# Performance work log

Measured on AMD Instinct MI355X. Metric: run time of the kernel, lower is better.

Reference implementation:

```python
import jax, jax.numpy as jnp
import numpy as np
import math

B, T, D, H, V, L = 8, 512, 128, 512, 50257, 8
DT = 1.0
RAW_INIT = math.log(math.expm1(1.0))  # so softplus(raw) == 1.0


def setup_inputs() -> dict:
    key = jax.random.key(0)
    ks = jax.random.split(key, 8)
    x = jax.random.randint(ks[0], (B, T), 0, V)
    E = jax.random.normal(ks[1], (V, D), jnp.float32) * 0.02
    P = jax.random.normal(ks[2], (T, D), jnp.float32) * 0.01
    W0 = jax.random.normal(ks[3], (2 * D, H), jnp.float32) * 0.02
    W1 = jax.random.normal(ks[4], (H, H), jnp.float32) * 0.02
    W2 = jax.random.normal(ks[5], (H, H), jnp.float32) * 0.02
    W3 = jax.random.normal(ks[6], (H, 1), jnp.float32) * 0.002
    return {
        'x': x, 'E': E, 'P': P,
        'W0': W0, 'b0': jnp.zeros((H,), jnp.float32),
        'W1': W1, 'b1': jnp.zeros((H,), jnp.float32),
        'W2': W2, 'b2': jnp.zeros((H,), jnp.float32),
        'W3': W3, 'b3': jnp.zeros((1,), jnp.float32),
        'raw_m_bias': jnp.asarray(RAW_INIT, jnp.float32),
        'raw_gamma': jnp.asarray(RAW_INIT, jnp.float32),
    }


def causal_cumulative_mean(h):
    t = h.shape[1]
    denom = jnp.arange(1, t + 1, dtype=h.dtype)[None, :, None]
    return jnp.cumsum(h, axis=1) / denom


def mlp_energy_sum(xi, h, W0, b0, W1, b1, W2, b2, W3, b3):
    z = jnp.concatenate([xi, h], axis=-1)  # (B,T,2D)
    z = jax.nn.gelu(z @ W0 + b0, approximate=False)
    z = jax.nn.gelu(z @ W1 + b1, approximate=False)
    z = jax.nn.gelu(z @ W2 + b2, approximate=False)
    return jnp.sum(z @ W3 + b3)


def reference(x, E, P, W0, b0, W1, b1, W2, b2, W3, b3, raw_m_bias, raw_gamma):
    emb = E[x] + P[None, :T]  # (B,T,D)
    gamma = jax.nn.softplus(raw_gamma)
    m = jax.nn.softplus(raw_m_bias) + 0.001  # global mass
    h = emb
    v = jnp.zeros_like(h)
    for _ in range(L):
        # causal_force=True: xi built from detached h
        xi = causal_cumulative_mean(jax.lax.stop_gradient(h))
        grad_V = jax.grad(
            lambda hh: mlp_energy_sum(xi, hh, W0, b0, W1, b1, W2, b2, W3, b3)
        )(h)
        f = -grad_V
        v = (v + DT * f / m) / (1.0 + DT * gamma)
        h = h + DT * v
    logits = jnp.einsum('btd,vd->btv', h, E)  # (B,T,V)
    return logits
```

## Files before the change

### kernel.cpp

```cpp
#include <hip/hip_runtime.h>
#include <hip/hip_bf16.h>

typedef __attribute__((ext_vector_type(8))) short short8;
typedef __attribute__((ext_vector_type(4))) float f32x4;
typedef unsigned char u8;

#define DEV static __device__ __forceinline__

DEV void gelu_pair(float x, float& z, float& dz){
  float ax = fabsf(x)*0.70710678118654752f;
  float e  = __expf(-ax*ax);
  float t  = __fdividef(1.0f, 1.0f + 0.3275911f*ax);
  float poly = t*(0.254829592f + t*(-0.284496736f + t*(1.421413741f +
               t*(-1.453152027f + t*1.061405429f))));
  float erfv = 1.0f - poly*e;
  erfv = x < 0.0f ? -erfv : erfv;
  float cdf = 0.5f*(1.0f + erfv);
  z  = x*cdf;
  dz = cdf + x*0.39894228040143268f*e;
}
DEV float dgelu_f(float x){ float zz, dz; gelu_pair(x, zz, dz); return dz; }
DEV float softplus_f(float x){ return log1pf(expf(x)); }
DEV void store_f4_a4(float* p, f32x4 v){ __builtin_memcpy(p, &v, 16); }

DEV void gload_lds16(const __hip_bfloat16* g, __hip_bfloat16* l){
  __builtin_amdgcn_global_load_lds((const __attribute__((address_space(1))) void*)g,
                                   (__attribute__((address_space(3))) void*)l, 16, 0, 0);
}

DEV u8 f2fp8(float f){
  int r = __builtin_amdgcn_cvt_pk_fp8_f32(f, f, 0, false);
  return (u8)(r & 0xff);
}
DEV unsigned pk4_fp8(float a, float b, float c, float d){
  int r = __builtin_amdgcn_cvt_pk_fp8_f32(a, b, 0, false);
  r = __builtin_amdgcn_cvt_pk_fp8_f32(c, d, r, true);
  return (unsigned)r;
}

DEV unsigned pack2bf(float a, float b){
  __hip_bfloat16 ba = __float2bfloat16(a), bb = __float2bfloat16(b);
  unsigned short ua, ub;
  __builtin_memcpy(&ua, &ba, 2); __builtin_memcpy(&ub, &bb, 2);
  return (unsigned)ua | ((unsigned)ub << 16);
}
DEV float unp_lo(unsigned u){ union{unsigned x; float f;} c; c.x = u << 16; return c.f; }
DEV float unp_hi(unsigned u){ union{unsigned x; float f;} c; c.x = u & 0xffff0000u; return c.f; }

#define SW    32.0f
#define SZC   32.0f
#define SZ1   256.0f
#define SZ2   1024.0f
#define SG3   256.0f
#define INV1  (1.0f/1024.0f)
#define INV2  (1.0f/8192.0f)
#define INV3  (1.0f/32768.0f)
#define INV4  (1.0f/8192.0f)
#define EN4   0.125f
#define INV5  (1.0f/32768.0f)
#define EN5   0.125f
#define INV6  (1.0f/131072.0f)

__global__ __launch_bounds__(512) void embed_k(const int* __restrict__ x,
                        const float* __restrict__ E, const float* __restrict__ P,
                        float* __restrict__ h, float* __restrict__ S){
  int bid = blockIdx.x;
  int row = threadIdx.x >> 5;
  int q   = threadIdx.x & 31;
  int tok = bid*16 + row;
  int t   = tok & 511;
  int id  = x[tok];
  float4 e4 = ((const float4*)E)[(size_t)id*32 + q];
  float4 p4 = ((const float4*)P)[(size_t)t*32 + q];
  float4 val; val.x=e4.x+p4.x; val.y=e4.y+p4.y; val.z=e4.z+p4.z; val.w=e4.w+p4.w;
  ((float4*)h)[(size_t)tok*32 + q] = val;
  __shared__ float4 ps[16][32];
  ps[row][q] = val;
  __syncthreads();
  if (row==0){
    float4 s = ps[0][q];
    #pragma unroll
    for (int r=1;r<16;r++){
      float4 t4 = ps[r][q];
      s.x+=t4.x; s.y+=t4.y; s.z+=t4.z; s.w+=t4.w;
    }
    ((float4*)S)[(size_t)bid*32 + q] = s;
  }
}

__global__ void convw_k(const float* __restrict__ W0, const float* __restrict__ W1,
                        const float* __restrict__ W2,
                        u8* __restrict__ W0T, u8* __restrict__ W1T,
                        u8* __restrict__ W2T, u8* __restrict__ W2b,
                        u8* __restrict__ W1b, u8* __restrict__ W0h){
  int i = blockIdx.x*256 + threadIdx.x;
  if (i < 131072){
    int e=i&7, n=(i>>3)&511, kk=i>>12; int k=(kk>>2)*32+(kk&3)*8+e;
    W0T[i]=f2fp8(SW*W0[(size_t)k*512+n]);
  } else if (i < 393216){
    int j=i-131072; int e=j&7, n=(j>>3)&511, kk=j>>12; int k=(kk>>2)*32+(kk&3)*8+e;
    W1T[j]=f2fp8(SW*W1[(size_t)k*512+n]);
  } else if (i < 655360){
    int j=i-393216; int e=j&7, n=(j>>3)&511, kk=j>>12; int k=(kk>>2)*32+(kk&3)*8+e;
    W2T[j]=f2fp8(SW*W2[(size_t)k*512+n]);
  } else if (i < 917504){
    int j=i-655360; int e=j&7, n=(j>>3)&511, kk=j>>12; int k=(kk>>2)*32+(kk&3)*8+e;
    W2b[j]=f2fp8(SW*W2[(size_t)n*512+k]);
  } else if (i < 1179648){
    int j=i-917504; int e=j&7, n=(j>>3)&511, kk=j>>12; int k=(kk>>2)*32+(kk&3)*8+e;
    W1b[j]=f2fp8(SW*W1[(size_t)n*512+k]);
  } else if (i < 1245184){
    int j=i-1179648; int e=j&7, n=(j>>3)&127, kk=j>>10; int k=(kk>>2)*32+(kk&3)*8+e;
    W0h[j]=f2fp8(SW*W0[(size_t)(128+n)*512+k]);
  }
}
__global__ void conv_c4_k(const float* __restrict__ W, __hip_bfloat16* __restrict__ Wb, int n4){
  int i = blockIdx.x*256 + threadIdx.x;
  if (i < n4){
    float4 f = ((const float4*)W)[i];
    Wb[4*i+0]=__float2bfloat16(f.x);
    Wb[4*i+1]=__float2bfloat16(f.y);
    Wb[4*i+2]=__float2bfloat16(f.z);
    Wb[4*i+3]=__float2bfloat16(f.w);
  }
}

struct LayerP {
  const u8 *W0T,*W1T,*W2T,*W2b,*W1b,*W0h;
  const float *b0,*b1,*b2,*W3;
  float *v, *h; __hip_bfloat16* hbf;
  const float* Sprev; float* Snext;
  const float *rawm,*rawg;
  int first, last;
};

template<int KSTEPS, int NW, int NF>
DEV void wpre(const u8* __restrict__ Wt, int nbase, int r16, int g, int rot,
              long (&bb)[6][NF]){
  const u8* wp = Wt + ((size_t)g*NW + nbase + r16)*8;
  #pragma unroll
  for (int d=0; d<5; d++){
    if (d < KSTEPS){
      int dd = (d + rot) & (KSTEPS-1);
      #pragma unroll
      for (int f=0; f<NF; f++)
        bb[d][f] = *(const long*)&wp[((size_t)dd*4*NW + (size_t)f*16)*8];
    }
  }
}

template<int KSTEPS, int NW, int NF>
DEV void gphase(const u8* __restrict__ Wt,
                const u8* __restrict__ zin,
                int nbase, int r16, int g, int rot, f32x4 (&acc)[NF],
                long (&bb)[6][NF]){
  #pragma unroll
  for (int f=0;f<NF;f++) acc[f] = (f32x4){0.f,0.f,0.f,0.f};
  const u8* wp = Wt + ((size_t)g*NW + nbase + r16)*8;
  #pragma unroll
  for (int s=0; s<KSTEPS; s++){
    if (s+5 < KSTEPS){
      int ss5 = (s + 5 + rot) & (KSTEPS-1);
      const u8* wn = wp + (size_t)ss5*4*NW*8;
      #pragma unroll
      for (int f=0; f<NF; f++)
        bb[(s+5)%6][f] = *(const long*)&wn[(size_t)f*128];
    }
    int ss = (s + rot) & (KSTEPS-1);
    long a = *(const long*)&zin[(ss*4+g)*128 + r16*8];
    #pragma unroll
    for (int f=0; f<NF; f++)
      acc[f] = __builtin_amdgcn_mfma_f32_16x16x32_fp8_fp8(a, bb[s%6][f], acc[f],0,0,0);
  }
}

__global__ __launch_bounds__(1024,4) void layer_k(LayerP p){
  __shared__ __align__(16) u8 sZ[2][8192];
  __shared__ float4 psum[16][32];
  __shared__ float4 psumC[16][32];
  const int tid = threadIdx.x;
  const int w = tid >> 6, lane = tid & 63;
  const int r16 = lane & 15, g = lane >> 4;
  const int rb = blockIdx.x;
  const int nb = w*32;
  const int rot = (rb >> 3) & 15;

  long bb[6][2];

  wpre<8,512,2>(p.W0T, nb, r16, g, rot, bb);
  float vr[4] = {0.f,0.f,0.f,0.f}, hr[4] = {0.f,0.f,0.f,0.f};
  float im = 0.f, fac = 0.f;
  if (w < 8){
    const int col = w*16 + r16;
    #pragma unroll
    for (int j=0;j<4;j++){
      size_t o = ((size_t)rb*16 + g*4 + j)*128 + col;
      hr[j] = p.h[o];
      vr[j] = p.first ? 0.f : p.v[o];
    }
    im  = INV6/(softplus_f(p.rawm[0]) + 0.001f);
    fac = 1.0f/(1.0f + softplus_f(p.rawg[0]));
  }

  if (tid < 512){
    const int row = tid >> 5;
    const int lane32 = tid & 31;
    const int b = rb >> 5, c = rb & 31;
    const float4* S4 = (const float4*)(p.Sprev + (size_t)b*32*128) + lane32;
    float4 part = {0.f,0.f,0.f,0.f};
    if (row < c){
      float4 t = S4[(size_t)row*32];
      part.x+=t.x; part.y+=t.y; part.z+=t.z; part.w+=t.w;
    }
    if (row+16 < c){
      float4 t = S4[(size_t)(row+16)*32];
      part.x+=t.x; part.y+=t.y; part.z+=t.z; part.w+=t.w;
    }
    float4 myrow = ((const float4*)(p.h + (size_t)rb*16*128))[(size_t)row*32 + lane32];
    psum[row][lane32]  = myrow;
    psumC[row][lane32] = part;
    __syncthreads();
    float4 pfx = {0.f,0.f,0.f,0.f};
    #pragma unroll
    for (int r=0;r<16;r++){
      float4 t = psumC[r][lane32];
      pfx.x+=t.x; pfx.y+=t.y; pfx.z+=t.z; pfx.w+=t.w;
    }
    #pragma unroll
    for (int rr=0; rr<15; rr++){
      float4 t = psum[rr][lane32];
      float sel = rr < row ? 1.0f : 0.0f;
      pfx.x += sel*t.x; pfx.y += sel*t.y; pfx.z += sel*t.z; pfx.w += sel*t.w;
    }
    pfx.x+=myrow.x; pfx.y+=myrow.y; pfx.z+=myrow.z; pfx.w+=myrow.w;
    float inv32 = SZC/(float)(c*16 + row + 1);
    const int d0 = lane32*4;
    unsigned ux = pk4_fp8(pfx.x*inv32, pfx.y*inv32, pfx.z*inv32, pfx.w*inv32);
    unsigned uh = pk4_fp8(myrow.x*SZC, myrow.y*SZC, myrow.z*SZC, myrow.w*SZC);
    *(unsigned*)&sZ[0][(d0>>3)*128      + row*8 + (d0&7)] = ux;
    *(unsigned*)&sZ[0][(16+(d0>>3))*128 + row*8 + (d0&7)] = uh;
  } else {
    __syncthreads();
  }
  __syncthreads();

  f32x4 acc[2];
  unsigned g1p[2][2], g2p[2][2];

  gphase<8,512,2>(p.W0T, sZ[0], nb, r16, g, rot, acc, bb);
  wpre<16,512,2>(p.W1T, nb, r16, g, rot, bb);
  #pragma unroll
  for (int f=0; f<2; f++){
    int n = nb + f*16 + r16;
    float bias = p.b0[n];
    #pragma unroll
    for (int jp=0; jp<2; jp++){
      float z0, dz0, z1v, dz1;
      gelu_pair(acc[f][2*jp]*INV1   + bias, z0,  dz0);
      gelu_pair(acc[f][2*jp+1]*INV1 + bias, z1v, dz1);
      g1p[f][jp] = pack2bf(dz0, dz1);
      sZ[1][(n>>3)*128 + (g*4+2*jp)*8   + (n&7)] = f2fp8(z0*SZ1);
      sZ[1][(n>>3)*128 + (g*4+2*jp+1)*8 + (n&7)] = f2fp8(z1v*SZ1);
    }
  }
  __syncthreads();

  gphase<16,512,2>(p.W1T, sZ[1], nb, r16, g, rot, acc, bb);
  wpre<16,512,2>(p.W2T, nb, r16, g, rot, bb);
  #pragma unroll
  for (int f=0; f<2; f++){
    int n = nb + f*16 + r16;
    float bias = p.b1[n];
    #pragma unroll
    for (int jp=0; jp<2; jp++){
      float z0, dz0, z1v, dz1;
      gelu_pair(acc[f][2*jp]*INV2   + bias, z0,  dz0);
      gelu_pair(acc[f][2*jp+1]*INV2 + bias, z1v, dz1);
      g2p[f][jp] = pack2bf(dz0, dz1);
      sZ[0][(n>>3)*128 + (g*4+2*jp)*8   + (n&7)] = f2fp8(z0*SZ2);
      sZ[0][(n>>3)*128 + (g*4+2*jp+1)*8 + (n&7)] = f2fp8(z1v*SZ2);
    }
  }
  __syncthreads();

  gphase<16,512,2>(p.W2T, sZ[0], nb, r16, g, rot, acc, bb);
  wpre<16,512,2>(p.W2b, nb, r16, g, rot, bb);
  #pragma unroll
  for (int f=0; f<2; f++){
    int n = nb + f*16 + r16;
    float bias = p.b2[n];
    float w3s = p.W3[n]*SG3;
    #pragma unroll
    for (int j=0;j<4;j++){
      float xx = acc[f][j]*INV3 + bias;
      sZ[1][(n>>3)*128 + (g*4+j)*8 + (n&7)] = f2fp8(w3s*dgelu_f(xx));
    }
  }
  __syncthreads();

  gphase<16,512,2>(p.W2b, sZ[1], nb, r16, g, rot, acc, bb);
  wpre<16,512,2>(p.W1b, nb, r16, g, rot, bb);
  #pragma unroll
  for (int f=0; f<2; f++){
    int n = nb + f*16 + r16;
    #pragma unroll
    for (int jp=0; jp<2; jp++){
      float gv0 = unp_lo(g2p[f][jp]), gv1 = unp_hi(g2p[f][jp]);
      sZ[0][(n>>3)*128 + (g*4+2*jp)*8   + (n&7)] = f2fp8(acc[f][2*jp]*gv0*EN4);
      sZ[0][(n>>3)*128 + (g*4+2*jp+1)*8 + (n&7)] = f2fp8(acc[f][2*jp+1]*gv1*EN4);
    }
  }
  __syncthreads();

  gphase<16,512,2>(p.W1b, sZ[0], nb, r16, g, rot, acc, bb);
  long bbF[6][1];
  if (w < 8) wpre<16,128,1>(p.W0h, w*16, r16, g, rot, bbF);
  #pragma unroll
  for (int f=0; f<2; f++){
    int n = nb + f*16 + r16;
    #pragma unroll
    for (int jp=0; jp<2; jp++){
      float gv0 = unp_lo(g1p[f][jp]), gv1 = unp_hi(g1p[f][jp]);
      sZ[1][(n>>3)*128 + (g*4+2*jp)*8   + (n&7)] = f2fp8(acc[f][2*jp]*gv0*EN5);
      sZ[1][(n>>3)*128 + (g*4+2*jp+1)*8 + (n&7)] = f2fp8(acc[f][2*jp+1]*gv1*EN5);
    }
  }
  __syncthreads();

  if (w < 8){
    f32x4 accF[1];
    gphase<16,128,1>(p.W0h, sZ[1], w*16, r16, g, rot, accF, bbF);
    int col = w*16 + r16;
    float hs = 0.f;
    #pragma unroll
    for (int j=0;j<4;j++){
      int row = g*4 + j;
      size_t o = ((size_t)rb*16 + row)*128 + col;
      float nv = (vr[j] - accF[0][j]*im)*fac;
      float nh = hr[j] + nv;
      if (!p.last){ p.v[o] = nv; p.h[o] = nh; }
      else        { p.hbf[o] = __float2bfloat16(nh); }
      hs += nh;
    }
    if (!p.last){
      hs += __shfl_xor(hs, 16);
      hs += __shfl_xor(hs, 32);
      if (g==0) p.Snext[(size_t)rb*128 + col] = hs;
    }
  }
}

__global__ __launch_bounds__(256,4) void logits_k(const __hip_bfloat16* __restrict__ A,
                                                  const __hip_bfloat16* __restrict__ Bt,
                                                  float* __restrict__ out){
  constexpr int V = 50257;
  __shared__ __align__(16) __hip_bfloat16 sA[128*64];
  __shared__ __align__(16) __hip_bfloat16 sB[128*64];
  const int tid = threadIdx.x, lane = tid & 63, wave = tid >> 6;
  const int wg = ((blockIdx.x & 7) * 1572) + (blockIdx.x >> 3);
  const int mt = wg & 31, nt = wg >> 5;
  const int m0 = mt*128, n0 = nt*128;
  const int wm = (wave>>1)*64, wn = (wave&1)*64;
  const int r16 = lane & 15, g = lane >> 4;
  const int srow = tid >> 3;
  const int scol = ((tid & 7) ^ (srow & 7)) * 8;
  const int sx = (r16 & 7) * 8;
  f32x4 zero = {0.f,0.f,0.f,0.f};
  f32x4 acc[4][4];
  #pragma unroll
  for (int i=0;i<4;i++){ acc[i][0]=zero; acc[i][1]=zero; acc[i][2]=zero; acc[i][3]=zero; }

  auto stageA = [&](int ks){
    #pragma unroll
    for (int i=0;i<4;i++)
      gload_lds16(A + (size_t)(m0 + i*32 + srow)*128 + ks*64 + scol,
                  &sA[i*2048 + wave*512]);
  };
  auto stageB = [&](int ks){
    #pragma unroll
    for (int i=0;i<4;i++){
      int r = n0 + i*32 + srow; if (r > V-1) r = V-1;
      gload_lds16(Bt + (size_t)r*128 + ks*64 + scol,
                  &sB[i*2048 + wave*512]);
    }
  };
  stageA(0); stageB(0);
  __syncthreads();
  #pragma unroll
  for (int ks=0; ks<2; ks++){
    #pragma unroll
    for (int kk=0; kk<2; kk++){
      const int ko = kk*32 + g*8;
      short8 a[4], b[4];
      #pragma unroll
      for (int ti=0; ti<4; ti++) a[ti] = *(const short8*)&sA[(wm + ti*16 + r16)*64 + (ko ^ sx)];
      #pragma unroll
      for (int tj=0; tj<4; tj++) b[tj] = *(const short8*)&sB[(wn + tj*16 + r16)*64 + (ko ^ sx)];
      #pragma unroll
      for (int tb=0; tb<4; tb++)
        #pragma unroll
        for (int ta=0; ta<4; ta++)
          acc[tb][ta] = __builtin_amdgcn_mfma_f32_16x16x32_bf16(b[tb],a[ta],acc[tb][ta],0,0,0);
    }
    if (ks==0){
      __syncthreads();
      stageA(1); stageB(1);
      __syncthreads();
    }
  }
  #pragma unroll
  for (int tb=0; tb<4; tb++){
    #pragma unroll
    for (int ta=0; ta<4; ta++){
      int row = m0 + wm + ta*16 + r16;
      int n   = n0 + wn + tb*16 + g*4;
      f32x4 c = acc[tb][ta];
      float* po = out + (size_t)row*V + n;
      if (n + 3 < V){
        store_f4_a4(po, c);
      } else {
        #pragma unroll
        for (int j=0;j<4;j++) if (n+j < V) po[j] = c[j];
      }
    }
  }
}

extern "C" void kernel_launch(void* const* d_in, const int* in_sizes, int n_in,
                              void* d_out, int out_size, void* d_ws, size_t ws_size,
                              hipStream_t stream){
  const int*   x    = (const int*)  d_in[0];
  const float* E    = (const float*)d_in[1];
  const float* P    = (const float*)d_in[2];
  const float* W0   = (const float*)d_in[3];
  const float* b0   = (const float*)d_in[4];
  const float* W1   = (const float*)d_in[5];
  const float* b1   = (const float*)d_in[6];
  const float* W2   = (const float*)d_in[7];
  const float* b2   = (const float*)d_in[8];
  const float* W3   = (const float*)d_in[9];
  const float* rawm = (const float*)d_in[11];
  const float* rawg = (const float*)d_in[12];

  constexpr int B=8, T=512, D=128, H=512, V=50257, L=8;
  const int M = B*T;

  char* w = (char*)d_ws;
  auto alloc = [&](size_t bytes)->char*{ char* r = w; w += (bytes + 255) & ~(size_t)255; return r; };
  float* h            = (float*)alloc((size_t)M*D*4);
  float* v            = (float*)alloc((size_t)M*D*4);
  __hip_bfloat16* hbf = (__hip_bfloat16*)alloc((size_t)M*D*2);
  float* S0           = (float*)alloc((size_t)B*32*128*4);
  float* S1           = (float*)alloc((size_t)B*32*128*4);
  u8* W0T             = (u8*)alloc((size_t)131072);
  u8* W1T             = (u8*)alloc((size_t)262144);
  u8* W2T             = (u8*)alloc((size_t)262144);
  u8* W2b             = (u8*)alloc((size_t)262144);
  u8* W1b             = (u8*)alloc((size_t)262144);
  u8* W0h             = (u8*)alloc((size_t)65536);
  __hip_bfloat16* Ebf = (__hip_bfloat16*)alloc((size_t)V*D*2);

  convw_k  <<<4864, 256, 0, stream>>>(W0, W1, W2, W0T, W1T, W2T, W2b, W1b, W0h);
  conv_c4_k<<<(V*D/4+255)/256, 256, 0, stream>>>(E, Ebf, V*D/4);
  embed_k<<<M/16, 512, 0, stream>>>(x, E, P, h, S0);

  LayerP lp{};
  lp.W0T=W0T; lp.W1T=W1T; lp.W2T=W2T; lp.W2b=W2b; lp.W1b=W1b; lp.W0h=W0h;
  lp.b0=b0; lp.b1=b1; lp.b2=b2; lp.W3=W3;
  lp.v=v; lp.h=h; lp.hbf=hbf; lp.rawm=rawm; lp.rawg=rawg;

  for (int l=0; l<L; l++){
    lp.Sprev = (l&1) ? S1 : S0;
    lp.Snext = (l&1) ? S0 : S1;
    lp.first = (l==0) ? 1 : 0;
    lp.last  = (l==L-1) ? 1 : 0;
    layer_k<<<M/16, 1024, 0, stream>>>(lp);
  }
  logits_k<<<12576, 256, 0, stream>>>(hbf, Ebf, (float*)d_out);
}
```

Before: 540.7 us.

## Fuse embedding and all layers into one persistent kernel with grid barrier

Replaces the embed kernel and the eight per-layer launches with a single persistent kernel of 256 blocks. The blocks synchronise between layers through an atomic grid barrier and keep h and v resident in shared memory instead of round-tripping them through global memory. This removes launch gaps and global h/v traffic. It relies on all 256 blocks being co-resident, otherwise the barrier deadlocks, and it adds spin-wait cost at each barrier.

```diff
diff --git a/kernel.cpp b/kernel.cpp
--- a/kernel.cpp
+++ b/kernel.cpp
@@ -55,45 +55,18 @@
 #define INV1  (1.0f/1024.0f)
 #define INV2  (1.0f/8192.0f)
 #define INV3  (1.0f/32768.0f)
-#define INV4  (1.0f/8192.0f)
 #define EN4   0.125f
-#define INV5  (1.0f/32768.0f)
 #define EN5   0.125f
 #define INV6  (1.0f/131072.0f)
-
-__global__ __launch_bounds__(512) void embed_k(const int* __restrict__ x,
-                        const float* __restrict__ E, const float* __restrict__ P,
-                        float* __restrict__ h, float* __restrict__ S){
-  int bid = blockIdx.x;
-  int row = threadIdx.x >> 5;
-  int q   = threadIdx.x & 31;
-  int tok = bid*16 + row;
-  int t   = tok & 511;
-  int id  = x[tok];
-  float4 e4 = ((const float4*)E)[(size_t)id*32 + q];
-  float4 p4 = ((const float4*)P)[(size_t)t*32 + q];
-  float4 val; val.x=e4.x+p4.x; val.y=e4.y+p4.y; val.z=e4.z+p4.z; val.w=e4.w+p4.w;
-  ((float4*)h)[(size_t)tok*32 + q] = val;
-  __shared__ float4 ps[16][32];
-  ps[row][q] = val;
-  __syncthreads();
-  if (row==0){
-    float4 s = ps[0][q];
-    #pragma unroll
-    for (int r=1;r<16;r++){
-      float4 t4 = ps[r][q];
-      s.x+=t4.x; s.y+=t4.y; s.z+=t4.z; s.w+=t4.w;
-    }
-    ((float4*)S)[(size_t)bid*32 + q] = s;
-  }
-}
 
 __global__ void convw_k(const float* __restrict__ W0, const float* __restrict__ W1,
                         const float* __restrict__ W2,
                         u8* __restrict__ W0T, u8* __restrict__ W1T,
                         u8* __restrict__ W2T, u8* __restrict__ W2b,
-                        u8* __restrict__ W1b, u8* __restrict__ W0h){
+                        u8* __restrict__ W1b, u8* __restrict__ W0h,
+                        int* __restrict__ bar){
   int i = blockIdx.x*256 + threadIdx.x;
+  if (i == 0) bar[0] = 0;
   if (i < 131072){
     int e=i&7, n=(i>>3)&511, kk=i>>12; int k=(kk>>2)*32+(kk&3)*8+e;
     W0T[i]=f2fp8(SW*W0[(size_t)k*512+n]);
@@ -125,14 +98,26 @@
   }
 }
 
-struct LayerP {
+struct MegaP {
+  const int* x; const float* E; const float* P;
   const u8 *W0T,*W1T,*W2T,*W2b,*W1b,*W0h;
   const float *b0,*b1,*b2,*W3;
-  float *v, *h; __hip_bfloat16* hbf;
-  const float* Sprev; float* Snext;
+  __hip_bfloat16* hbf;
+  float *S0, *S1;
   const float *rawm,*rawg;
-  int first, last;
+  int* bar;
 };
+
+DEV void grid_bar(int* bar, int target){
+  __syncthreads();
+  if (threadIdx.x == 0){
+    __threadfence();
+    __hip_atomic_fetch_add(bar, 1, __ATOMIC_ACQ_REL, __HIP_MEMORY_SCOPE_AGENT);
+    while (__hip_atomic_load(bar, __ATOMIC_ACQUIRE, __HIP_MEMORY_SCOPE_AGENT) < target)
+      __builtin_amdgcn_s_sleep(2);
+  }
+  __syncthreads();
+}
 
 template<int KSTEPS, int NW, int NF>
 DEV void wpre(const u8* __restrict__ Wt, int nbase, int r16, int g, int rot,
@@ -174,178 +159,215 @@
   }
 }
 
-__global__ __launch_bounds__(1024,4) void layer_k(LayerP p){
+__global__ __launch_bounds__(1024,4) void mega_k(MegaP p){
   __shared__ __align__(16) u8 sZ[2][8192];
   __shared__ float4 psum[16][32];
   __shared__ float4 psumC[16][32];
+  __shared__ float  sVv[2048];
   const int tid = threadIdx.x;
   const int w = tid >> 6, lane = tid & 63;
   const int r16 = lane & 15, g = lane >> 4;
   const int rb = blockIdx.x;
   const int nb = w*32;
   const int rot = (rb >> 3) & 15;
+  const int bt = rb >> 5, c = rb & 31;
 
   long bb[6][2];
-
   wpre<8,512,2>(p.W0T, nb, r16, g, rot, bb);
-  float vr[4] = {0.f,0.f,0.f,0.f}, hr[4] = {0.f,0.f,0.f,0.f};
-  float im = 0.f, fac = 0.f;
-  if (w < 8){
-    const int col = w*16 + r16;
-    #pragma unroll
-    for (int j=0;j<4;j++){
-      size_t o = ((size_t)rb*16 + g*4 + j)*128 + col;
-      hr[j] = p.h[o];
-      vr[j] = p.first ? 0.f : p.v[o];
-    }
-    im  = INV6/(softplus_f(p.rawm[0]) + 0.001f);
-    fac = 1.0f/(1.0f + softplus_f(p.rawg[0]));
-  }
+
+  const float im  = INV6/(softplus_f(p.rawm[0]) + 0.001f);
+  const float fac = 1.0f/(1.0f + softplus_f(p.rawg[0]));
 
   if (tid < 512){
-    const int row = tid >> 5;
-    const int lane32 = tid & 31;
-    const int b = rb >> 5, c = rb & 31;
-    const float4* S4 = (const float4*)(p.Sprev + (size_t)b*32*128) + lane32;
-    float4 part = {0.f,0.f,0.f,0.f};
-    if (row < c){
-      float4 t = S4[(size_t)row*32];
-      part.x+=t.x; part.y+=t.y; part.z+=t.z; part.w+=t.w;
-    }
-    if (row+16 < c){
-      float4 t = S4[(size_t)(row+16)*32];
-      part.x+=t.x; part.y+=t.y; part.z+=t.z; part.w+=t.w;
-    }
-    float4 myrow = ((const float4*)(p.h + (size_t)rb*16*128))[(size_t)row*32 + lane32];
-    psum[row][lane32]  = myrow;
-    psumC[row][lane32] = part;
-    __syncthreads();
-    float4 pfx = {0.f,0.f,0.f,0.f};
-    #pragma unroll
-    for (int r=0;r<16;r++){
-      float4 t = psumC[r][lane32];
-      pfx.x+=t.x; pfx.y+=t.y; pfx.z+=t.z; pfx.w+=t.w;
-    }
-    #pragma unroll
-    for (int rr=0; rr<15; rr++){
-      float4 t = psum[rr][lane32];
-      float sel = rr < row ? 1.0f : 0.0f;
-      pfx.x += sel*t.x; pfx.y += sel*t.y; pfx.z += sel*t.z; pfx.w += sel*t.w;
-    }
-    pfx.x+=myrow.x; pfx.y+=myrow.y; pfx.z+=myrow.z; pfx.w+=myrow.w;
-    float inv32 = SZC/(float)(c*16 + row + 1);
-    const int d0 = lane32*4;
-    unsigned ux = pk4_fp8(pfx.x*inv32, pfx.y*inv32, pfx.z*inv32, pfx.w*inv32);
-    unsigned uh = pk4_fp8(myrow.x*SZC, myrow.y*SZC, myrow.z*SZC, myrow.w*SZC);
-    *(unsigned*)&sZ[0][(d0>>3)*128      + row*8 + (d0&7)] = ux;
-    *(unsigned*)&sZ[0][(16+(d0>>3))*128 + row*8 + (d0&7)] = uh;
-  } else {
-    __syncthreads();
+    int row = tid >> 5, lane32 = tid & 31;
+    int tok = rb*16 + row, t = tok & 511;
+    int id = p.x[tok];
+    float4 e4 = ((const float4*)p.E)[(size_t)id*32 + lane32];
+    float4 p4 = ((const float4*)p.P)[(size_t)t*32 + lane32];
+    float4 val; val.x=e4.x+p4.x; val.y=e4.y+p4.y; val.z=e4.z+p4.z; val.w=e4.w+p4.w;
+    psum[row][lane32] = val;
   }
   __syncthreads();
+  if (tid < 32){
+    float4 s = psum[0][tid];
+    #pragma unroll
+    for (int r=1;r<16;r++){
+      float4 t4 = psum[r][tid];
+      s.x+=t4.x; s.y+=t4.y; s.z+=t4.z; s.w+=t4.w;
+    }
+    float* d = p.S0 + (size_t)rb*128 + tid*4;
+    __hip_atomic_store(d+0, s.x, __ATOMIC_RELAXED, __HIP_MEMORY_SCOPE_AGENT);
+    __hip_atomic_store(d+1, s.y, __ATOMIC_RELAXED, __HIP_MEMORY_SCOPE_AGENT);
+    __hip_atomic_store(d+2, s.z, __ATOMIC_RELAXED, __HIP_MEMORY_SCOPE_AGENT);
+    __hip_atomic_store(d+3, s.w, __ATOMIC_RELAXED, __HIP_MEMORY_SCOPE_AGENT);
+  }
+  grid_bar(p.bar, 256);
 
   f32x4 acc[2];
   unsigned g1p[2][2], g2p[2][2];
 
-  gphase<8,512,2>(p.W0T, sZ[0], nb, r16, g, rot, acc, bb);
-  wpre<16,512,2>(p.W1T, nb, r16, g, rot, bb);
-  #pragma unroll
-  for (int f=0; f<2; f++){
-    int n = nb + f*16 + r16;
-    float bias = p.b0[n];
-    #pragma unroll
-    for (int jp=0; jp<2; jp++){
-      float z0, dz0, z1v, dz1;
-      gelu_pair(acc[f][2*jp]*INV1   + bias, z0,  dz0);
-      gelu_pair(acc[f][2*jp+1]*INV1 + bias, z1v, dz1);
-      g1p[f][jp] = pack2bf(dz0, dz1);
-      sZ[1][(n>>3)*128 + (g*4+2*jp)*8   + (n&7)] = f2fp8(z0*SZ1);
-      sZ[1][(n>>3)*128 + (g*4+2*jp+1)*8 + (n&7)] = f2fp8(z1v*SZ1);
-    }
-  }
-  __syncthreads();
-
-  gphase<16,512,2>(p.W1T, sZ[1], nb, r16, g, rot, acc, bb);
-  wpre<16,512,2>(p.W2T, nb, r16, g, rot, bb);
-  #pragma unroll
-  for (int f=0; f<2; f++){
-    int n = nb + f*16 + r16;
-    float bias = p.b1[n];
-    #pragma unroll
-    for (int jp=0; jp<2; jp++){
-      float z0, dz0, z1v, dz1;
-      gelu_pair(acc[f][2*jp]*INV2   + bias, z0,  dz0);
-      gelu_pair(acc[f][2*jp+1]*INV2 + bias, z1v, dz1);
-      g2p[f][jp] = pack2bf(dz0, dz1);
-      sZ[0][(n>>3)*128 + (g*4+2*jp)*8   + (n&7)] = f2fp8(z0*SZ2);
-      sZ[0][(n>>3)*128 + (g*4+2*jp+1)*8 + (n&7)] = f2fp8(z1v*SZ2);
-    }
-  }
-  __syncthreads();
-
-  gphase<16,512,2>(p.W2T, sZ[0], nb, r16, g, rot, acc, bb);
-  wpre<16,512,2>(p.W2b, nb, r16, g, rot, bb);
-  #pragma unroll
-  for (int f=0; f<2; f++){
-    int n = nb + f*16 + r16;
-    float bias = p.b2[n];
-    float w3s = p.W3[n]*SG3;
-    #pragma unroll
-    for (int j=0;j<4;j++){
-      float xx = acc[f][j]*INV3 + bias;
-      sZ[1][(n>>3)*128 + (g*4+j)*8 + (n&7)] = f2fp8(w3s*dgelu_f(xx));
-    }
-  }
-  __syncthreads();
-
-  gphase<16,512,2>(p.W2b, sZ[1], nb, r16, g, rot, acc, bb);
-  wpre<16,512,2>(p.W1b, nb, r16, g, rot, bb);
-  #pragma unroll
-  for (int f=0; f<2; f++){
-    int n = nb + f*16 + r16;
-    #pragma unroll
-    for (int jp=0; jp<2; jp++){
-      float gv0 = unp_lo(g2p[f][jp]), gv1 = unp_hi(g2p[f][jp]);
-      sZ[0][(n>>3)*128 + (g*4+2*jp)*8   + (n&7)] = f2fp8(acc[f][2*jp]*gv0*EN4);
-      sZ[0][(n>>3)*128 + (g*4+2*jp+1)*8 + (n&7)] = f2fp8(acc[f][2*jp+1]*gv1*EN4);
-    }
-  }
-  __syncthreads();
-
-  gphase<16,512,2>(p.W1b, sZ[0], nb, r16, g, rot, acc, bb);
-  long bbF[6][1];
-  if (w < 8) wpre<16,128,1>(p.W0h, w*16, r16, g, rot, bbF);
-  #pragma unroll
-  for (int f=0; f<2; f++){
-    int n = nb + f*16 + r16;
-    #pragma unroll
-    for (int jp=0; jp<2; jp++){
-      float gv0 = unp_lo(g1p[f][jp]), gv1 = unp_hi(g1p[f][jp]);
-      sZ[1][(n>>3)*128 + (g*4+2*jp)*8   + (n&7)] = f2fp8(acc[f][2*jp]*gv0*EN5);
-      sZ[1][(n>>3)*128 + (g*4+2*jp+1)*8 + (n&7)] = f2fp8(acc[f][2*jp+1]*gv1*EN5);
-    }
-  }
-  __syncthreads();
-
-  if (w < 8){
-    f32x4 accF[1];
-    gphase<16,128,1>(p.W0h, sZ[1], w*16, r16, g, rot, accF, bbF);
-    int col = w*16 + r16;
-    float hs = 0.f;
-    #pragma unroll
-    for (int j=0;j<4;j++){
-      int row = g*4 + j;
-      size_t o = ((size_t)rb*16 + row)*128 + col;
-      float nv = (vr[j] - accF[0][j]*im)*fac;
-      float nh = hr[j] + nv;
-      if (!p.last){ p.v[o] = nv; p.h[o] = nh; }
-      else        { p.hbf[o] = __float2bfloat16(nh); }
-      hs += nh;
-    }
-    if (!p.last){
-      hs += __shfl_xor(hs, 16);
-      hs += __shfl_xor(hs, 32);
-      if (g==0) p.Snext[(size_t)rb*128 + col] = hs;
+  #pragma unroll 1
+  for (int l=0; l<8; l++){
+    const float* Sp = (l&1) ? p.S1 : p.S0;
+    float*       Sn = (l&1) ? p.S0 : p.S1;
+
+    if (tid < 512){
+      const int row = tid >> 5;
+      const int lane32 = tid & 31;
+      float4 part = {0.f,0.f,0.f,0.f};
+      const float* Sb = Sp + (size_t)bt*32*128 + lane32*4;
+      if (row < c){
+        const float* q4 = Sb + (size_t)row*128;
+        part.x += __hip_atomic_load(q4+0, __ATOMIC_RELAXED, __HIP_MEMORY_SCOPE_AGENT);
+        part.y += __hip_atomic_load(q4+1, __ATOMIC_RELAXED, __HIP_MEMORY_SCOPE_AGENT);
+        part.z += __hip_atomic_load(q4+2, __ATOMIC_RELAXED, __HIP_MEMORY_SCOPE_AGENT);
+        part.w += __hip_atomic_load(q4+3, __ATOMIC_RELAXED, __HIP_MEMORY_SCOPE_AGENT);
+      }
+      if (row+16 < c){
+        const float* q4 = Sb + (size_t)(row+16)*128;
+        part.x += __hip_atomic_load(q4+0, __ATOMIC_RELAXED, __HIP_MEMORY_SCOPE_AGENT);
+        part.y += __hip_atomic_load(q4+1, __ATOMIC_RELAXED, __HIP_MEMORY_SCOPE_AGENT);
+        part.z += __hip_atomic_load(q4+2, __ATOMIC_RELAXED, __HIP_MEMORY_SCOPE_AGENT);
+        part.w += __hip_atomic_load(q4+3, __ATOMIC_RELAXED, __HIP_MEMORY_SCOPE_AGENT);
+      }
+      float4 myrow = psum[row][lane32];
+      psumC[row][lane32] = part;
+      __syncthreads();
+      float4 pfx = {0.f,0.f,0.f,0.f};
+      #pragma unroll
+      for (int r=0;r<16;r++){
+        float4 t = psumC[r][lane32];
+        pfx.x+=t.x; pfx.y+=t.y; pfx.z+=t.z; pfx.w+=t.w;
+      }
+      #pragma unroll
+      for (int rr=0; rr<15; rr++){
+        float4 t = psum[rr][lane32];
+        float sel = rr < row ? 1.0f : 0.0f;
+        pfx.x += sel*t.x; pfx.y += sel*t.y; pfx.z += sel*t.z; pfx.w += sel*t.w;
+      }
+      pfx.x+=myrow.x; pfx.y+=myrow.y; pfx.z+=myrow.z; pfx.w+=myrow.w;
+      float inv32 = SZC/(float)(c*16 + row + 1);
+      const int d0 = lane32*4;
+      unsigned ux = pk4_fp8(pfx.x*inv32, pfx.y*inv32, pfx.z*inv32, pfx.w*inv32);
+      unsigned uh = pk4_fp8(myrow.x*SZC, myrow.y*SZC, myrow.z*SZC, myrow.w*SZC);
+      *(unsigned*)&sZ[0][(d0>>3)*128      + row*8 + (d0&7)] = ux;
+      *(unsigned*)&sZ[0][(16+(d0>>3))*128 + row*8 + (d0&7)] = uh;
+    } else {
+      __syncthreads();
+    }
+    __syncthreads();
+
+    gphase<8,512,2>(p.W0T, sZ[0], nb, r16, g, rot, acc, bb);
+    wpre<16,512,2>(p.W1T, nb, r16, g, rot, bb);
+    #pragma unroll
+    for (int f=0; f<2; f++){
+      int n = nb + f*16 + r16;
+      float bias = p.b0[n];
+      #pragma unroll
+      for (int jp=0; jp<2; jp++){
+        float z0, dz0, z1v, dz1;
+        gelu_pair(acc[f][2*jp]*INV1   + bias, z0,  dz0);
+        gelu_pair(acc[f][2*jp+1]*INV1 + bias, z1v, dz1);
+        g1p[f][jp] = pack2bf(dz0, dz1);
+        sZ[1][(n>>3)*128 + (g*4+2*jp)*8   + (n&7)] = f2fp8(z0*SZ1);
+        sZ[1][(n>>3)*128 + (g*4+2*jp+1)*8 + (n&7)] = f2fp8(z1v*SZ1);
+      }
+    }
+    __syncthreads();
+
+    gphase<16,512,2>(p.W1T, sZ[1], nb, r16, g, rot, acc, bb);
+    wpre<16,512,2>(p.W2T, nb, r16, g, rot, bb);
+    #pragma unroll
+    for (int f=0; f<2; f++){
+      int n = nb + f*16 + r16;
+      float bias = p.b1[n];
+      #pragma unroll
+      for (int jp=0; jp<2; jp++){
+        float z0, dz0, z1v, dz1;
+        gelu_pair(acc[f][2*jp]*INV2   + bias, z0,  dz0);
+        gelu_pair(acc[f][2*jp+1]*INV2 + bias, z1v, dz1);
+        g2p[f][jp] = pack2bf(dz0, dz1);
+        sZ[0][(n>>3)*128 + (g*4+2*jp)*8   + (n&7)] = f2fp8(z0*SZ2);
+        sZ[0][(n>>3)*128 + (g*4+2*jp+1)*8 + (n&7)] = f2fp8(z1v*SZ2);
+      }
+    }
+    __syncthreads();
+
+    gphase<16,512,2>(p.W2T, sZ[0], nb, r16, g, rot, acc, bb);
+    wpre<16,512,2>(p.W2b, nb, r16, g, rot, bb);
+    #pragma unroll
+    for (int f=0; f<2; f++){
+      int n = nb + f*16 + r16;
+      float bias = p.b2[n];
+      float w3s = p.W3[n]*SG3;
+      #pragma unroll
+      for (int j=0;j<4;j++){
+        float xx = acc[f][j]*INV3 + bias;
+        sZ[1][(n>>3)*128 + (g*4+j)*8 + (n&7)] = f2fp8(w3s*dgelu_f(xx));
+      }
+    }
+    __syncthreads();
+
+    gphase<16,512,2>(p.W2b, sZ[1], nb, r16, g, rot, acc, bb);
+    wpre<16,512,2>(p.W1b, nb, r16, g, rot, bb);
+    #pragma unroll
+    for (int f=0; f<2; f++){
+      int n = nb + f*16 + r16;
+      #pragma unroll
+      for (int jp=0; jp<2; jp++){
+        float gv0 = unp_lo(g2p[f][jp]), gv1 = unp_hi(g2p[f][jp]);
+        sZ[0][(n>>3)*128 + (g*4+2*jp)*8   + (n&7)] = f2fp8(acc[f][2*jp]*gv0*EN4);
+        sZ[0][(n>>3)*128 + (g*4+2*jp+1)*8 + (n&7)] = f2fp8(acc[f][2*jp+1]*gv1*EN4);
+      }
+    }
+    __syncthreads();
+
+    gphase<16,512,2>(p.W1b, sZ[0], nb, r16, g, rot, acc, bb);
+    long bbF[6][1];
+    if (w < 8) wpre<16,128,1>(p.W0h, w*16, r16, g, rot, bbF);
+    #pragma unroll
+    for (int f=0; f<2; f++){
+      int n = nb + f*16 + r16;
+      #pragma unroll
+      for (int jp=0; jp<2; jp++){
+        float gv0 = unp_lo(g1p[f][jp]), gv1 = unp_hi(g1p[f][jp]);
+        sZ[1][(n>>3)*128 + (g*4+2*jp)*8   + (n&7)] = f2fp8(acc[f][2*jp]*gv0*EN5);
+        sZ[1][(n>>3)*128 + (g*4+2*jp+1)*8 + (n&7)] = f2fp8(acc[f][2*jp+1]*gv1*EN5);
+      }
+    }
+    __syncthreads();
+
+    if (w < 8){
+      f32x4 accF[1];
+      gphase<16,128,1>(p.W0h, sZ[1], w*16, r16, g, rot, accF, bbF);
+      int col = w*16 + r16;
+      float hs = 0.f;
+      #pragma unroll
+      for (int j=0;j<4;j++){
+        int row = g*4 + j;
+        float vold = (l==0) ? 0.f : sVv[row*128 + col];
+        float hold = ((const float*)psum)[row*128 + col];
+        float nv = (vold - accF[0][j]*im)*fac;
+        float nh = hold + nv;
+        if (l < 7){
+          sVv[row*128 + col] = nv;
+          ((float*)psum)[row*128 + col] = nh;
+        } else {
+          p.hbf[((size_t)rb*16 + row)*128 + col] = __float2bfloat16(nh);
+        }
+        hs += nh;
+      }
+      if (l < 7){
+        hs += __shfl_xor(hs, 16);
+        hs += __shfl_xor(hs, 32);
+        if (g==0)
+          __hip_atomic_store(Sn + (size_t)rb*128 + col, hs,
+                             __ATOMIC_RELAXED, __HIP_MEMORY_SCOPE_AGENT);
+      }
+    }
+    if (l < 7){
+      wpre<8,512,2>(p.W0T, nb, r16, g, rot, bb);
+      grid_bar(p.bar, 256*(l+2));
     }
   }
 }
@@ -442,13 +464,11 @@
   const float* rawm = (const float*)d_in[11];
   const float* rawg = (const float*)d_in[12];
 
-  constexpr int B=8, T=512, D=128, H=512, V=50257, L=8;
+  constexpr int B=8, T=512, D=128, V=50257;
   const int M = B*T;
 
   char* w = (char*)d_ws;
   auto alloc = [&](size_t bytes)->char*{ char* r = w; w += (bytes + 255) & ~(size_t)255; return r; };
-  float* h            = (float*)alloc((size_t)M*D*4);
-  float* v            = (float*)alloc((size_t)M*D*4);
   __hip_bfloat16* hbf = (__hip_bfloat16*)alloc((size_t)M*D*2);
   float* S0           = (float*)alloc((size_t)B*32*128*4);
   float* S1           = (float*)alloc((size_t)B*32*128*4);
@@ -459,22 +479,18 @@
   u8* W1b             = (u8*)alloc((size_t)262144);
   u8* W0h             = (u8*)alloc((size_t)65536);
   __hip_bfloat16* Ebf = (__hip_bfloat16*)alloc((size_t)V*D*2);
-
-  convw_k  <<<4864, 256, 0, stream>>>(W0, W1, W2, W0T, W1T, W2T, W2b, W1b, W0h);
+  int* bar            = (int*)alloc(256);
+
+  convw_k  <<<4864, 256, 0, stream>>>(W0, W1, W2, W0T, W1T, W2T, W2b, W1b, W0h, bar);
   conv_c4_k<<<(V*D/4+255)/256, 256, 0, stream>>>(E, Ebf, V*D/4);
-  embed_k<<<M/16, 512, 0, stream>>>(x, E, P, h, S0);
-
-  LayerP lp{};
-  lp.W0T=W0T; lp.W1T=W1T; lp.W2T=W2T; lp.W2b=W2b; lp.W1b=W1b; lp.W0h=W0h;
-  lp.b0=b0; lp.b1=b1; lp.b2=b2; lp.W3=W3;
-  lp.v=v; lp.h=h; lp.hbf=hbf; lp.rawm=rawm; lp.rawg=rawg;
-
-  for (int l=0; l<L; l++){
-    lp.Sprev = (l&1) ? S1 : S0;
-    lp.Snext = (l&1) ? S0 : S1;
-    lp.first = (l==0) ? 1 : 0;
-    lp.last  = (l==L-1) ? 1 : 0;
-    layer_k<<<M/16, 1024, 0, stream>>>(lp);
-  }
+
+  MegaP mp{};
+  mp.x=x; mp.E=E; mp.P=P;
+  mp.W0T=W0T; mp.W1T=W1T; mp.W2T=W2T; mp.W2b=W2b; mp.W1b=W1b; mp.W0h=W0h;
+  mp.b0=b0; mp.b1=b1; mp.b2=b2; mp.W3=W3;
+  mp.hbf=hbf; mp.S0=S0; mp.S1=S1;
+  mp.rawm=rawm; mp.rawg=rawg; mp.bar=bar;
+  mega_k<<<256, 1024, 0, stream>>>(mp);
+
   logits_k<<<12576, 256, 0, stream>>>(hbf, Ebf, (float*)d_out);
 }
```

Measured after the change: 1.444 ms. 2.67x slower.

## Halve rows per layer block and widen each wave to four column fragments

Applied to the files above, without the earlier changes.

The fused layer kernel now handles 8 token rows per block with 512 threads instead of 16 rows with 1024 threads. Each wave computes 64 output columns (four MFMA fragments) rather than 32. The prefix-sum chunking, embed kernel and partial-sum buffers are resized to 8-row chunks. This doubles the block count to give the scheduler more independent work. In exchange, the 16-row MFMA tiles are only half filled, and the weights are streamed twice as often across blocks.

```diff
diff --git a/kernel.cpp b/kernel.cpp
--- a/kernel.cpp
+++ b/kernel.cpp
@@ -55,32 +55,30 @@
 #define INV1  (1.0f/1024.0f)
 #define INV2  (1.0f/8192.0f)
 #define INV3  (1.0f/32768.0f)
-#define INV4  (1.0f/8192.0f)
 #define EN4   0.125f
-#define INV5  (1.0f/32768.0f)
 #define EN5   0.125f
 #define INV6  (1.0f/131072.0f)
 
-__global__ __launch_bounds__(512) void embed_k(const int* __restrict__ x,
+__global__ __launch_bounds__(256) void embed_k(const int* __restrict__ x,
                         const float* __restrict__ E, const float* __restrict__ P,
                         float* __restrict__ h, float* __restrict__ S){
   int bid = blockIdx.x;
   int row = threadIdx.x >> 5;
   int q   = threadIdx.x & 31;
-  int tok = bid*16 + row;
+  int tok = bid*8 + row;
   int t   = tok & 511;
   int id  = x[tok];
   float4 e4 = ((const float4*)E)[(size_t)id*32 + q];
   float4 p4 = ((const float4*)P)[(size_t)t*32 + q];
   float4 val; val.x=e4.x+p4.x; val.y=e4.y+p4.y; val.z=e4.z+p4.z; val.w=e4.w+p4.w;
   ((float4*)h)[(size_t)tok*32 + q] = val;
-  __shared__ float4 ps[16][32];
+  __shared__ float4 ps[8][32];
   ps[row][q] = val;
   __syncthreads();
   if (row==0){
     float4 s = ps[0][q];
     #pragma unroll
-    for (int r=1;r<16;r++){
+    for (int r=1;r<8;r++){
       float4 t4 = ps[r][q];
       s.x+=t4.x; s.y+=t4.y; s.z+=t4.z; s.w+=t4.w;
     }
@@ -174,66 +172,64 @@
   }
 }
 
-__global__ __launch_bounds__(1024,4) void layer_k(LayerP p){
+__global__ __launch_bounds__(512,4) void layer_k(LayerP p){
   __shared__ __align__(16) u8 sZ[2][8192];
-  __shared__ float4 psum[16][32];
-  __shared__ float4 psumC[16][32];
+  __shared__ float4 psum[8][32];
+  __shared__ float4 psumC[8][32];
   const int tid = threadIdx.x;
   const int w = tid >> 6, lane = tid & 63;
   const int r16 = lane & 15, g = lane >> 4;
   const int rb = blockIdx.x;
-  const int nb = w*32;
+  const int nb = w*64;
   const int rot = (rb >> 3) & 15;
 
-  long bb[6][2];
-
-  wpre<8,512,2>(p.W0T, nb, r16, g, rot, bb);
+  long bb[6][4];
+
+  wpre<8,512,4>(p.W0T, nb, r16, g, rot, bb);
   float vr[4] = {0.f,0.f,0.f,0.f}, hr[4] = {0.f,0.f,0.f,0.f};
-  float im = 0.f, fac = 0.f;
-  if (w < 8){
-    const int col = w*16 + r16;
+  const int col = w*16 + r16;
+  if (g < 2){
     #pragma unroll
     for (int j=0;j<4;j++){
-      size_t o = ((size_t)rb*16 + g*4 + j)*128 + col;
+      size_t o = ((size_t)rb*8 + g*4 + j)*128 + col;
       hr[j] = p.h[o];
       vr[j] = p.first ? 0.f : p.v[o];
     }
-    im  = INV6/(softplus_f(p.rawm[0]) + 0.001f);
-    fac = 1.0f/(1.0f + softplus_f(p.rawg[0]));
-  }
-
-  if (tid < 512){
+  }
+  const float im  = INV6/(softplus_f(p.rawm[0]) + 0.001f);
+  const float fac = 1.0f/(1.0f + softplus_f(p.rawg[0]));
+
+  if (tid < 256){
     const int row = tid >> 5;
     const int lane32 = tid & 31;
-    const int b = rb >> 5, c = rb & 31;
-    const float4* S4 = (const float4*)(p.Sprev + (size_t)b*32*128) + lane32;
+    const int bt = rb >> 6, c = rb & 63;
+    const float4* S4 = (const float4*)(p.Sprev + (size_t)bt*64*128) + lane32;
     float4 part = {0.f,0.f,0.f,0.f};
-    if (row < c){
-      float4 t = S4[(size_t)row*32];
-      part.x+=t.x; part.y+=t.y; part.z+=t.z; part.w+=t.w;
-    }
-    if (row+16 < c){
-      float4 t = S4[(size_t)(row+16)*32];
-      part.x+=t.x; part.y+=t.y; part.z+=t.z; part.w+=t.w;
-    }
-    float4 myrow = ((const float4*)(p.h + (size_t)rb*16*128))[(size_t)row*32 + lane32];
+    #pragma unroll
+    for (int k=0;k<8;k++){
+      if (row + 8*k < c){
+        float4 t = S4[(size_t)(row+8*k)*32];
+        part.x+=t.x; part.y+=t.y; part.z+=t.z; part.w+=t.w;
+      }
+    }
+    float4 myrow = ((const float4*)(p.h + (size_t)rb*8*128))[(size_t)row*32 + lane32];
     psum[row][lane32]  = myrow;
     psumC[row][lane32] = part;
     __syncthreads();
     float4 pfx = {0.f,0.f,0.f,0.f};
     #pragma unroll
-    for (int r=0;r<16;r++){
+    for (int r=0;r<8;r++){
       float4 t = psumC[r][lane32];
       pfx.x+=t.x; pfx.y+=t.y; pfx.z+=t.z; pfx.w+=t.w;
     }
     #pragma unroll
-    for (int rr=0; rr<15; rr++){
+    for (int rr=0; rr<7; rr++){
       float4 t = psum[rr][lane32];
       float sel = rr < row ? 1.0f : 0.0f;
       pfx.x += sel*t.x; pfx.y += sel*t.y; pfx.z += sel*t.z; pfx.w += sel*t.w;
     }
     pfx.x+=myrow.x; pfx.y+=myrow.y; pfx.z+=myrow.z; pfx.w+=myrow.w;
-    float inv32 = SZC/(float)(c*16 + row + 1);
+    float inv32 = SZC/(float)(c*8 + row + 1);
     const int d0 = lane32*4;
     unsigned ux = pk4_fp8(pfx.x*inv32, pfx.y*inv32, pfx.z*inv32, pfx.w*inv32);
     unsigned uh = pk4_fp8(myrow.x*SZC, myrow.y*SZC, myrow.z*SZC, myrow.w*SZC);
@@ -244,13 +240,13 @@
   }
   __syncthreads();
 
-  f32x4 acc[2];
-  unsigned g1p[2][2], g2p[2][2];
-
-  gphase<8,512,2>(p.W0T, sZ[0], nb, r16, g, rot, acc, bb);
-  wpre<16,512,2>(p.W1T, nb, r16, g, rot, bb);
-  #pragma unroll
-  for (int f=0; f<2; f++){
+  f32x4 acc[4];
+  unsigned g1p[4][2], g2p[4][2];
+
+  gphase<8,512,4>(p.W0T, sZ[0], nb, r16, g, rot, acc, bb);
+  wpre<16,512,4>(p.W1T, nb, r16, g, rot, bb);
+  #pragma unroll
+  for (int f=0; f<4; f++){
     int n = nb + f*16 + r16;
     float bias = p.b0[n];
     #pragma unroll
@@ -265,10 +261,10 @@
   }
   __syncthreads();
 
-  gphase<16,512,2>(p.W1T, sZ[1], nb, r16, g, rot, acc, bb);
-  wpre<16,512,2>(p.W2T, nb, r16, g, rot, bb);
-  #pragma unroll
-  for (int f=0; f<2; f++){
+  gphase<16,512,4>(p.W1T, sZ[1], nb, r16, g, rot, acc, bb);
+  wpre<16,512,4>(p.W2T, nb, r16, g, rot, bb);
+  #pragma unroll
+  for (int f=0; f<4; f++){
     int n = nb + f*16 + r16;
     float bias = p.b1[n];
     #pragma unroll
@@ -283,10 +279,10 @@
   }
   __syncthreads();
 
-  gphase<16,512,2>(p.W2T, sZ[0], nb, r16, g, rot, acc, bb);
-  wpre<16,512,2>(p.W2b, nb, r16, g, rot, bb);
-  #pragma unroll
-  for (int f=0; f<2; f++){
+  gphase<16,512,4>(p.W2T, sZ[0], nb, r16, g, rot, acc, bb);
+  wpre<16,512,4>(p.W2b, nb, r16, g, rot, bb);
+  #pragma unroll
+  for (int f=0; f<4; f++){
     int n = nb + f*16 + r16;
     float bias = p.b2[n];
     float w3s = p.W3[n]*SG3;
@@ -298,10 +294,10 @@
   }
   __syncthreads();
 
-  gphase<16,512,2>(p.W2b, sZ[1], nb, r16, g, rot, acc, bb);
-  wpre<16,512,2>(p.W1b, nb, r16, g, rot, bb);
-  #pragma unroll
-  for (int f=0; f<2; f++){
+  gphase<16,512,4>(p.W2b, sZ[1], nb, r16, g, rot, acc, bb);
+  wpre<16,512,4>(p.W1b, nb, r16, g, rot, bb);
+  #pragma unroll
+  for (int f=0; f<4; f++){
     int n = nb + f*16 + r16;
     #pragma unroll
     for (int jp=0; jp<2; jp++){
@@ -312,11 +308,11 @@
   }
   __syncthreads();
 
-  gphase<16,512,2>(p.W1b, sZ[0], nb, r16, g, rot, acc, bb);
+  gphase<16,512,4>(p.W1b, sZ[0], nb, r16, g, rot, acc, bb);
   long bbF[6][1];
-  if (w < 8) wpre<16,128,1>(p.W0h, w*16, r16, g, rot, bbF);
-  #pragma unroll
-  for (int f=0; f<2; f++){
+  wpre<16,128,1>(p.W0h, w*16, r16, g, rot, bbF);
+  #pragma unroll
+  for (int f=0; f<4; f++){
     int n = nb + f*16 + r16;
     #pragma unroll
     for (int jp=0; jp<2; jp++){
@@ -327,24 +323,24 @@
   }
   __syncthreads();
 
-  if (w < 8){
+  {
     f32x4 accF[1];
     gphase<16,128,1>(p.W0h, sZ[1], w*16, r16, g, rot, accF, bbF);
-    int col = w*16 + r16;
     float hs = 0.f;
-    #pragma unroll
-    for (int j=0;j<4;j++){
-      int row = g*4 + j;
-      size_t o = ((size_t)rb*16 + row)*128 + col;
-      float nv = (vr[j] - accF[0][j]*im)*fac;
-      float nh = hr[j] + nv;
-      if (!p.last){ p.v[o] = nv; p.h[o] = nh; }
-      else        { p.hbf[o] = __float2bfloat16(nh); }
-      hs += nh;
+    if (g < 2){
+      #pragma unroll
+      for (int j=0;j<4;j++){
+        int row = g*4 + j;
+        size_t o = ((size_t)rb*8 + row)*128 + col;
+        float nv = (vr[j] - accF[0][j]*im)*fac;
+        float nh = hr[j] + nv;
+        if (!p.last){ p.v[o] = nv; p.h[o] = nh; }
+        else        { p.hbf[o] = __float2bfloat16(nh); }
+        hs += nh;
+      }
     }
     if (!p.last){
       hs += __shfl_xor(hs, 16);
-      hs += __shfl_xor(hs, 32);
       if (g==0) p.Snext[(size_t)rb*128 + col] = hs;
     }
   }
@@ -442,7 +438,7 @@
   const float* rawm = (const float*)d_in[11];
   const float* rawg = (const float*)d_in[12];
 
-  constexpr int B=8, T=512, D=128, H=512, V=50257, L=8;
+  constexpr int B=8, T=512, D=128, V=50257, L=8;
   const int M = B*T;
 
   char* w = (char*)d_ws;
@@ -450,8 +446,8 @@
   float* h            = (float*)alloc((size_t)M*D*4);
   float* v            = (float*)alloc((size_t)M*D*4);
   __hip_bfloat16* hbf = (__hip_bfloat16*)alloc((size_t)M*D*2);
-  float* S0           = (float*)alloc((size_t)B*32*128*4);
-  float* S1           = (float*)alloc((size_t)B*32*128*4);
+  float* S0           = (float*)alloc((size_t)512*128*4);
+  float* S1           = (float*)alloc((size_t)512*128*4);
   u8* W0T             = (u8*)alloc((size_t)131072);
   u8* W1T             = (u8*)alloc((size_t)262144);
   u8* W2T             = (u8*)alloc((size_t)262144);
@@ -462,7 +458,7 @@
 
   convw_k  <<<4864, 256, 0, stream>>>(W0, W1, W2, W0T, W1T, W2T, W2b, W1b, W0h);
   conv_c4_k<<<(V*D/4+255)/256, 256, 0, stream>>>(E, Ebf, V*D/4);
-  embed_k<<<M/16, 512, 0, stream>>>(x, E, P, h, S0);
+  embed_k<<<M/8, 256, 0, stream>>>(x, E, P, h, S0);
 
   LayerP lp{};
   lp.W0T=W0T; lp.W1T=W1T; lp.W2T=W2T; lp.W2b=W2b; lp.W1b=W1b; lp.W0h=W0h;
@@ -474,7 +470,7 @@
     lp.Snext = (l&1) ? S0 : S1;
     lp.first = (l==0) ? 1 : 0;
     lp.last  = (l==L-1) ? 1 : 0;
-    layer_k<<<M/16, 1024, 0, stream>>>(lp);
+    layer_k<<<M/8, 512, 0, stream>>>(lp);
   }
   logits_k<<<12576, 256, 0, stream>>>(hbf, Ebf, (float*)d_out);
 }
```

After: 725.5 us. 1.34x slower.
